# Optimization experiments

Hardware: AMD Instinct MI355X
Metric: run time of the kernel (lower is better)

The kernel has to match this reference:

```python
import jax, jax.numpy as jnp
import numpy as np

NUM_HEADS = 16


def setup_inputs() -> dict:
    key = jax.random.key(0)
    ks = jax.random.split(key, 9)
    B, N, C, R, T = 16, 1024, 1024, 64, 10
    s = 0.02
    x = jax.random.normal(ks[0], (B, N, C), dtype=jnp.float32)
    W_qkv = jax.random.normal(ks[1], (3 * C, C), dtype=jnp.float32) * s
    W_proj = jax.random.normal(ks[2], (C, C), dtype=jnp.float32) * s
    b_proj = jax.random.normal(ks[3], (C,), dtype=jnp.float32) * s
    A_k = jax.random.normal(ks[4], (T, R, C), dtype=jnp.float32) * s
    B_k = jax.random.normal(ks[5], (T, C, R), dtype=jnp.float32) * s
    A_v = jax.random.normal(ks[6], (T, R, C), dtype=jnp.float32) * s
    B_v = jax.random.normal(ks[7], (T, C, R), dtype=jnp.float32) * s
    return {"x": x, "W_qkv": W_qkv, "W_proj": W_proj, "b_proj": b_proj,
            "A_k": A_k, "B_k": B_k, "A_v": A_v, "B_v": B_v, "task": 4}


def reference(x, W_qkv, W_proj, b_proj, A_k, B_k, A_v, B_v, task):
    B, N, C = x.shape
    H = NUM_HEADS
    hd = C // H
    scale = hd ** (-0.5)

    # qkv projection: x @ W_qkv.T -> [B,N,3C] -> [3,B,H,N,hd]
    qkv = (x @ W_qkv.T).reshape(B, N, 3, H, hd).transpose(2, 0, 3, 1, 4)
    q, k, v = qkv[0], qkv[1], qkv[2]

    # merged LoRA weights: sum_{t<=task} B[t] @ A[t] -> [C, C]
    w_k = jnp.einsum('tcr,trd->cd', B_k[:task + 1], A_k[:task + 1])
    w_v = jnp.einsum('tcr,trd->cd', B_v[:task + 1], A_v[:task + 1])
    # F.linear(x, W) = x @ W.T ; reshape to [B,H,N,hd]
    dk = (x @ w_k.T).reshape(B, N, H, hd).transpose(0, 2, 1, 3)
    dv = (x @ w_v.T).reshape(B, N, H, hd).transpose(0, 2, 1, 3)
    k = k + dk
    v = v + dv

    attn = jax.nn.softmax(jnp.einsum('bhnd,bhmd->bhnm', q, k) * scale, axis=-1)
    out = jnp.einsum('bhnm,bhmd->bhnd', attn, v)
    out = out.transpose(0, 2, 1, 3).reshape(B, N, C)
    return out @ W_proj.T + b_proj
```

## Files before the change

kernel.cpp:

```cpp
#include <hip/hip_runtime.h>

typedef __attribute__((ext_vector_type(4))) float f32x4;
typedef __attribute__((ext_vector_type(8))) short s16x8;
typedef __attribute__((ext_vector_type(2))) unsigned int u32x2;
typedef __attribute__((ext_vector_type(4))) unsigned int u32x4;

#define LOG2E 1.44269504088896340736f

__device__ inline unsigned short f2b(float f) {
  unsigned int u = __float_as_uint(f);
  unsigned int r = (u + 0x7FFFu + ((u >> 16) & 1u)) >> 16;
  return (unsigned short)r;
}

__device__ inline unsigned int cvtpk_bf16(float lo, float hi) {
  unsigned int r;
  asm("v_cvt_pk_bf16_f32 %0, %1, %2" : "=v"(r) : "v"(lo), "v"(hi));
  return r;
}

__device__ inline void gload_lds16(const unsigned short* g, unsigned short* l) {
  __builtin_amdgcn_global_load_lds(
      (const __attribute__((address_space(1))) unsigned int*)g,
      (__attribute__((address_space(3))) unsigned int*)l, 16, 0, 0);
}

#define MFMA16(a, b, c) __builtin_amdgcn_mfma_f32_16x16x32_bf16((a), (b), (c), 0, 0, 0)

__global__ __launch_bounds__(256) void lora_and_cvt(const float* __restrict__ A_k,
                                                    const float* __restrict__ B_k,
                                                    const float* __restrict__ A_v,
                                                    const float* __restrict__ B_v,
                                                    float* __restrict__ wk,
                                                    float* __restrict__ wv,
                                                    const int* __restrict__ taskp,
                                                    const float* __restrict__ x,
                                                    const float* __restrict__ Wproj,
                                                    unsigned short* __restrict__ xb,
                                                    unsigned short* __restrict__ Wp) {
  __shared__ float Bs[64][65];
  __shared__ float As[64][65];
  const int blk = blockIdx.x;
  const int tid = threadIdx.x;
  if (blk >= 512) {
    int i = (blk - 512) * 256 + tid;
    const float* src;
    unsigned short* dst;
    int idx;
    if (i < 4194304) { idx = i; src = x; dst = xb; }
    else { idx = i - 4194304; src = Wproj; dst = Wp; }
    f32x4 v = ((const f32x4*)src)[idx];
    unsigned short o0 = f2b(v.x), o1 = f2b(v.y), o2 = f2b(v.z), o3 = f2b(v.w);
    unsigned long long pack = (unsigned long long)o0 | ((unsigned long long)o1 << 16) |
                              ((unsigned long long)o2 << 32) | ((unsigned long long)o3 << 48);
    ((unsigned long long*)dst)[idx] = pack;
    return;
  }
  const int kv = (blk >> 8) & 1;
  const float* A_ = kv ? A_v : A_k;
  const float* B_ = kv ? B_v : B_k;
  float* Wd = kv ? wv : wk;
  const int tile = blk & 255;
  const int c0 = (tile >> 4) * 64, d0 = (tile & 15) * 64;
  const int tx = tid & 15, ty = tid >> 4;
  const int T = *taskp + 1;
  float acc[4][4] = {};
  const int r = tid >> 2, cb = (tid & 3) * 16;
  for (int t = 0; t < T; ++t) {
    __syncthreads();
    const float* srcB = B_ + (size_t)t * 65536 + (size_t)(c0 + r) * 64 + cb;
    const float* srcA = A_ + (size_t)t * 65536 + (size_t)r * 1024 + d0 + cb;
#pragma unroll
    for (int j = 0; j < 16; j += 4) {
      f32x4 vb = *(const f32x4*)(srcB + j);
      Bs[r][cb + j] = vb.x; Bs[r][cb + j + 1] = vb.y;
      Bs[r][cb + j + 2] = vb.z; Bs[r][cb + j + 3] = vb.w;
      f32x4 va = *(const f32x4*)(srcA + j);
      As[r][cb + j] = va.x; As[r][cb + j + 1] = va.y;
      As[r][cb + j + 2] = va.z; As[r][cb + j + 3] = va.w;
    }
    __syncthreads();
#pragma unroll 8
    for (int rr = 0; rr < 64; ++rr) {
      float bv[4], av[4];
#pragma unroll
      for (int i2 = 0; i2 < 4; ++i2) bv[i2] = Bs[ty * 4 + i2][rr];
#pragma unroll
      for (int j = 0; j < 4; ++j) av[j] = As[rr][tx * 4 + j];
#pragma unroll
      for (int i2 = 0; i2 < 4; ++i2)
#pragma unroll
        for (int j = 0; j < 4; ++j) acc[i2][j] += bv[i2] * av[j];
    }
  }
#pragma unroll
  for (int i2 = 0; i2 < 4; ++i2)
#pragma unroll
    for (int j = 0; j < 4; ++j)
      Wd[(size_t)(c0 + ty * 4 + i2) * 1024 + d0 + tx * 4 + j] = acc[i2][j];
}

__global__ void build_wc(const float* __restrict__ Wqkv, const float* __restrict__ wk,
                         const float* __restrict__ wv, unsigned short* __restrict__ Wc) {
  int i = blockIdx.x * 256 + threadIdx.x;
  int e = i * 4;
  f32x4 v = *(const f32x4*)(Wqkv + e);
  int row = e >> 10;
  if (row >= 2048) {
    f32x4 d = *(const f32x4*)(wv + (e - 2097152));
    v = v + d;
  } else if (row >= 1024) {
    f32x4 d = *(const f32x4*)(wk + (e - 1048576));
    v = v + d;
  }
  unsigned short o0 = f2b(v.x), o1 = f2b(v.y), o2 = f2b(v.z), o3 = f2b(v.w);
  unsigned long long pack = (unsigned long long)o0 | ((unsigned long long)o1 << 16) |
                            ((unsigned long long)o2 << 32) | ((unsigned long long)o3 << 48);
  ((unsigned long long*)Wc)[i] = pack;
}

template <int OUT_BF16, int ADD_BIAS, int VFUSE>
__global__ __launch_bounds__(512, 1) void gemm256(const unsigned short* __restrict__ A,
                                                  const unsigned short* __restrict__ B,
                                                  void* __restrict__ Cout,
                                                  const float* __restrict__ bias,
                                                  unsigned short* __restrict__ Vt,
                                                  int M, int N, int K) {
  __shared__ unsigned short SM[65536];
  const int tid = threadIdx.x;
  const int w = tid >> 6, l = tid & 63;
  const int lr = l & 15, lg = l >> 4;
  const int wm = w >> 2, wn = w & 3;

  const int lin = blockIdx.y * gridDim.x + blockIdx.x;
  const int cpx = (gridDim.x * gridDim.y) >> 3;
  const int s = (lin & 7) * cpx + (lin >> 3);
  const int bx = s % gridDim.x, by = s / gridDim.x;

  const int r_st = tid >> 2;
  const int k_st = ((tid & 3) ^ ((tid >> 3) & 3)) << 3;
  const unsigned short* gA0 = A + (size_t)(by * 256 + r_st) * K + k_st;
  const unsigned short* gA1 = A + (size_t)(by * 256 + 128 + r_st) * K + k_st;
  const unsigned short* gB0 = B + (size_t)(bx * 256 + r_st) * K + k_st;
  const unsigned short* gB1 = B + (size_t)(bx * 256 + 128 + r_st) * K + k_st;
  const int wb = w * 512;

  const int fs = lr * 32 + ((lg ^ ((lr >> 1) & 3)) << 3);
  const int A0 = wm * 8192;
  const int B0 = 32768 + (wn >> 1) * 8192;
  const int nb = (wn & 1) * 4;

  f32x4 acc[8][4] = {};
  const int NT2 = K >> 7;

#define STA(bb, kt, kk)                                                          \
  gload_lds16(gA0 + (kt) * 64 + (kk) * 32, &SM[(bb) * 16384 + (kk) * 4096 + wb]); \
  gload_lds16(gA1 + (kt) * 64 + (kk) * 32, &SM[(bb) * 16384 + 8192 + (kk) * 4096 + wb]);
#define STB(bb, kt, kk)                                                                   \
  gload_lds16(gB0 + (kt) * 64 + (kk) * 32, &SM[32768 + (bb) * 16384 + (kk) * 4096 + wb]); \
  gload_lds16(gB1 + (kt) * 64 + (kk) * 32, &SM[32768 + (bb) * 16384 + 8192 + (kk) * 4096 + wb]);
#define PH_GATE                                            \
  __builtin_amdgcn_s_barrier();                            \
  asm volatile("s_waitcnt lgkmcnt(0)" ::: "memory");       \
  __builtin_amdgcn_sched_barrier(0);                       \
  __builtin_amdgcn_s_setprio(1);
#define PH_END                                             \
  __builtin_amdgcn_s_setprio(0);                           \
  __builtin_amdgcn_sched_barrier(0);                       \
  __builtin_amdgcn_s_barrier();
#define PH_END_VM                                          \
  __builtin_amdgcn_s_setprio(0);                           \
  __builtin_amdgcn_sched_barrier(0);                       \
  asm volatile("s_waitcnt vmcnt(6)" ::: "memory");         \
  __builtin_amdgcn_s_barrier();                            \
  __builtin_amdgcn_sched_barrier(0);

  STA(0, 0, 0); STB(0, 0, 0); STA(0, 0, 1); STB(0, 0, 1);
  STA(1, 1, 0); STB(1, 1, 0); STA(1, 1, 1);
  asm volatile("s_waitcnt vmcnt(6)" ::: "memory");
  __builtin_amdgcn_s_barrier();
  __builtin_amdgcn_sched_barrier(0);

  for (int it = 0; it < NT2; ++it) {
    const int kt1 = 2 * it + 1;
    const int st2 = (it < NT2 - 1) ? 2 * it + 2 : 2 * it;
    const int st3 = (it < NT2 - 1) ? 2 * it + 3 : 2 * it + 1;
    s16x8 af[8], bf[2];
#pragma unroll
    for (int m = 0; m < 8; ++m) af[m] = *(const s16x8*)&SM[A0 + m * 512 + fs];
#pragma unroll
    for (int j = 0; j < 2; ++j) bf[j] = *(const s16x8*)&SM[B0 + (nb + j) * 512 + fs];
    STB(1, kt1, 1);
    PH_GATE
#pragma unroll
    for (int m = 0; m < 8; ++m)
#pragma unroll
      for (int j = 0; j < 2; ++j) acc[m][j] = MFMA16(af[m], bf[j], acc[m][j]);
    PH_END
#pragma unroll
    for (int j = 0; j < 2; ++j) bf[j] = *(const s16x8*)&SM[B0 + (nb + 2 + j) * 512 + fs];
    STA(0, st2, 0);
    PH_GATE
#pragma unroll
    for (int m = 0; m < 8; ++m)
#pragma unroll
      for (int j = 0; j < 2; ++j) acc[m][2 + j] = MFMA16(af[m], bf[j], acc[m][2 + j]);
    PH_END
#pragma unroll
    for (int m = 0; m < 8; ++m) af[m] = *(const s16x8*)&SM[A0 + 4096 + m * 512 + fs];
#pragma unroll
    for (int j = 0; j < 2; ++j) bf[j] = *(const s16x8*)&SM[B0 + 4096 + (nb + j) * 512 + fs];
    STB(0, st2, 0);
    PH_GATE
#pragma unroll
    for (int m = 0; m < 8; ++m)
#pragma unroll
      for (int j = 0; j < 2; ++j) acc[m][j] = MFMA16(af[m], bf[j], acc[m][j]);
    PH_END
#pragma unroll
    for (int j = 0; j < 2; ++j) bf[j] = *(const s16x8*)&SM[B0 + 4096 + (nb + 2 + j) * 512 + fs];
    STA(0, st2, 1);
    PH_GATE
#pragma unroll
    for (int m = 0; m < 8; ++m)
#pragma unroll
      for (int j = 0; j < 2; ++j) acc[m][2 + j] = MFMA16(af[m], bf[j], acc[m][2 + j]);
    PH_END_VM
#pragma unroll
    for (int m = 0; m < 8; ++m) af[m] = *(const s16x8*)&SM[16384 + A0 + m * 512 + fs];
#pragma unroll
    for (int j = 0; j < 2; ++j) bf[j] = *(const s16x8*)&SM[16384 + B0 + (nb + j) * 512 + fs];
    STB(0, st2, 1);
    PH_GATE
#pragma unroll
    for (int m = 0; m < 8; ++m)
#pragma unroll
      for (int j = 0; j < 2; ++j) acc[m][j] = MFMA16(af[m], bf[j], acc[m][j]);
    PH_END
#pragma unroll
    for (int j = 0; j < 2; ++j) bf[j] = *(const s16x8*)&SM[16384 + B0 + (nb + 2 + j) * 512 + fs];
    STA(1, st3, 0);
    PH_GATE
#pragma unroll
    for (int m = 0; m < 8; ++m)
#pragma unroll
      for (int j = 0; j < 2; ++j) acc[m][2 + j] = MFMA16(af[m], bf[j], acc[m][2 + j]);
    PH_END
#pragma unroll
    for (int m = 0; m < 8; ++m) af[m] = *(const s16x8*)&SM[16384 + A0 + 4096 + m * 512 + fs];
#pragma unroll
    for (int j = 0; j < 2; ++j) bf[j] = *(const s16x8*)&SM[16384 + B0 + 4096 + (nb + j) * 512 + fs];
    STB(1, st3, 0);
    PH_GATE
#pragma unroll
    for (int m = 0; m < 8; ++m)
#pragma unroll
      for (int j = 0; j < 2; ++j) acc[m][j] = MFMA16(af[m], bf[j], acc[m][j]);
    PH_END
#pragma unroll
    for (int j = 0; j < 2; ++j) bf[j] = *(const s16x8*)&SM[16384 + B0 + 4096 + (nb + 2 + j) * 512 + fs];
    STA(1, st3, 1);
    PH_GATE
#pragma unroll
    for (int m = 0; m < 8; ++m)
#pragma unroll
      for (int j = 0; j < 2; ++j) acc[m][2 + j] = MFMA16(af[m], bf[j], acc[m][2 + j]);
    PH_END_VM
  }

  const int crow0 = by * 256 + wm * 128;
  const int ccol0 = bx * 256 + wn * 64;

  if (VFUSE) {
    unsigned short* Cq = (unsigned short*)Cout;
    if (bx < 8) {
      unsigned short* Cb = Cq + ((size_t)((ccol0 >> 10) & 1)) * 16777216;
#pragma unroll
      for (int m = 0; m < 8; ++m)
#pragma unroll
        for (int n = 0; n < 4; ++n)
#pragma unroll
          for (int rr = 0; rr < 4; ++rr) {
            int row = crow0 + m * 16 + lg * 4 + rr;
            int col = (ccol0 + n * 16 + lr) & 1023;
            Cb[(size_t)row * 1024 + col] = f2b(acc[m][n][rr]);
          }
    } else {
      asm volatile("s_waitcnt vmcnt(0)" ::: "memory");
      __syncthreads();
      unsigned int* T32 = (unsigned int*)SM;
      const int h0 = (bx - 8) * 4;
      const int bb = by >> 2;
      const int n_base = (by & 3) * 256;
#pragma unroll
      for (int hf = 0; hf < 2; ++hf) {
        if (wm == hf) {
#pragma unroll
          for (int m = 0; m < 8; ++m)
#pragma unroll
            for (int n = 0; n < 4; ++n) {
              int lcol = wn * 64 + n * 16 + lr;
              u32x2 pk;
              pk.x = (unsigned int)f2b(acc[m][n][0]) | ((unsigned int)f2b(acc[m][n][1]) << 16);
              pk.y = (unsigned int)f2b(acc[m][n][2]) | ((unsigned int)f2b(acc[m][n][3]) << 16);
              *(u32x2*)&T32[lcol * 68 + m * 8 + lg * 2] = pk;
            }
        }
        __syncthreads();
#pragma unroll
        for (int p = 0; p < 8; ++p) {
          int slot2 = p * 512 + tid;
          int d256 = slot2 >> 4;
          int ncq = (slot2 & 15) * 4;
          u32x4 v = *(const u32x4*)&T32[d256 * 68 + ncq];
          int hloc = d256 >> 6, d = d256 & 63;
          size_t dst = (size_t)(bb * 16 + h0 + hloc) * 65536 + (size_t)d * 1024 +
                       (n_base + hf * 128 + ncq * 2);
          *(u32x4*)&Vt[dst] = v;
        }
        __syncthreads();
      }
    }
  } else if (OUT_BF16) {
    unsigned short* C = (unsigned short*)Cout;
#pragma unroll
    for (int m = 0; m < 8; ++m)
#pragma unroll
      for (int n = 0; n < 4; ++n)
#pragma unroll
        for (int rr = 0; rr < 4; ++rr) {
          int row = crow0 + m * 16 + lg * 4 + rr;
          int col = ccol0 + n * 16 + lr;
          C[(size_t)row * N + col] = f2b(acc[m][n][rr]);
        }
  } else {
    float* C = (float*)Cout;
#pragma unroll
    for (int m = 0; m < 8; ++m)
#pragma unroll
      for (int n = 0; n < 4; ++n)
#pragma unroll
        for (int rr = 0; rr < 4; ++rr) {
          int row = crow0 + m * 16 + lg * 4 + rr;
          int col = ccol0 + n * 16 + lr;
          float b = ADD_BIAS ? bias[col] : 0.f;
          C[(size_t)row * N + col] = acc[m][n][rr] + b;
        }
  }
#undef STA
#undef STB
#undef PH_GATE
#undef PH_END
#undef PH_END_VM
}

__global__ __launch_bounds__(512) void attn_fwd(const unsigned short* __restrict__ Qb,
                                                const unsigned short* __restrict__ Kb,
                                                const unsigned short* __restrict__ vT,
                                                unsigned short* __restrict__ out) {
  const int tid = threadIdx.x;
  const int w = tid >> 6, l = tid & 63;
  const int lr = l & 15, lg = l >> 4;
  const int bid = blockIdx.x;
  const int g = (bid & 7) * 32 + (bid >> 5);
  const int qt2 = (bid >> 3) & 3;
  const int b = g >> 4, h = g & 15;

  __shared__ unsigned short Ks[2][4096];
  __shared__ unsigned short Vs[2][4096];
  __shared__ unsigned int Ps[8][576];

  const size_t base = (size_t)b * 1048576 + h * 64;
  const unsigned short* Qp = Qb + base;
  const unsigned short* Kp = Kb + base;
  const unsigned short* vTp = vT + (size_t)(b * 16 + h) * 65536;

  const float SSCALE = 0.125f * LOG2E;
  const int qb = qt2 * 256;
  s16x8 qf[2][2];
#pragma unroll
  for (int qg = 0; qg < 2; ++qg) {
    const int qrow = qb + qg * 128 + w * 16 + lr;
    qf[qg][0] = *(const s16x8*)(Qp + (size_t)qrow * 1024 + lg * 8);
    qf[qg][1] = *(const s16x8*)(Qp + (size_t)qrow * 1024 + 32 + lg * 8);
#pragma unroll
    for (int kk = 0; kk < 2; ++kk)
#pragma unroll
      for (int j = 0; j < 8; ++j) {
        float f = __uint_as_float(((unsigned int)(unsigned short)qf[qg][kk][j]) << 16) * SSCALE;
        qf[qg][kk][j] = (short)f2b(f);
      }
  }

  s16x8 ONES;
#pragma unroll
  for (int j = 0; j < 8; ++j) ONES[j] = (short)0x3F80;

  f32x4 o[2][4] = {};
  f32x4 o4[2] = {};

  const int srow = tid >> 3;
  const int csrc = (tid & 7) ^ (srow & 7);

  gload_lds16(Kp + (size_t)srow * 1024 + csrc * 8, &Ks[0][w * 512]);
  gload_lds16(vTp + (size_t)srow * 1024 + csrc * 8, &Vs[0][w * 512]);
  __syncthreads();

  for (int t = 0; t < 16; ++t) {
    const int cur = t & 1;
    if (t < 15) {
      const int kv1 = (t + 1) * 64;
      gload_lds16(Kp + (size_t)(kv1 + srow) * 1024 + csrc * 8, &Ks[cur ^ 1][w * 512]);
      gload_lds16(vTp + (size_t)srow * 1024 + kv1 + csrc * 8, &Vs[cur ^ 1][w * 512]);
    }
    const unsigned short* Kb_ = &Ks[cur][0];
    const unsigned short* Vb = &Vs[cur][0];

    f32x4 sc[2][4] = {};
    __builtin_amdgcn_s_setprio(1);
#pragma unroll
    for (int kk = 0; kk < 2; ++kk)
#pragma unroll
      for (int tt = 0; tt < 4; ++tt) {
        int krow = tt * 16 + lr;
        s16x8 kf = *(const s16x8*)&Kb_[krow * 64 + ((((kk * 32 + lg * 8) >> 3) ^ (krow & 7)) << 3)];
        sc[0][tt] = MFMA16(kf, qf[0][kk], sc[0][tt]);
        sc[1][tt] = MFMA16(kf, qf[1][kk], sc[1][tt]);
      }
    __builtin_amdgcn_s_setprio(0);

    s16x8 pf[2][2];
#pragma unroll
    for (int qg = 0; qg < 2; ++qg) {
      unsigned int* Pw = &Ps[w][0];
#pragma unroll
      for (int tt = 0; tt < 4; ++tt) {
        float p0 = exp2f(sc[qg][tt][0]);
        float p1 = exp2f(sc[qg][tt][1]);
        float p2 = exp2f(sc[qg][tt][2]);
        float p3 = exp2f(sc[qg][tt][3]);
        u32x2 pk;
        pk.x = cvtpk_bf16(p0, p1);
        pk.y = cvtpk_bf16(p2, p3);
        *(u32x2*)&Pw[lr * 36 + tt * 8 + lg * 2] = pk;
      }
      __builtin_amdgcn_sched_barrier(0);
#pragma unroll
      for (int kk = 0; kk < 2; ++kk) {
        u32x4 pu = *(const u32x4*)&Pw[lr * 36 + kk * 16 + lg * 4];
        pf[qg][kk] = __builtin_bit_cast(s16x8, pu);
      }
      __builtin_amdgcn_sched_barrier(0);
    }

#pragma unroll
    for (int kk = 0; kk < 2; ++kk) {
      __builtin_amdgcn_s_setprio(1);
      o4[0] = MFMA16(pf[0][kk], ONES, o4[0]);
      o4[1] = MFMA16(pf[1][kk], ONES, o4[1]);
#pragma unroll
      for (int dt = 0; dt < 4; ++dt) {
        int vrow = dt * 16 + lr;
        s16x8 vf = *(const s16x8*)&Vb[vrow * 64 + ((((kk * 32 + lg * 8) >> 3) ^ (vrow & 7)) << 3)];
        o[0][dt] = MFMA16(pf[0][kk], vf, o[0][dt]);
        o[1][dt] = MFMA16(pf[1][kk], vf, o[1][dt]);
      }
      __builtin_amdgcn_s_setprio(0);
    }
    __syncthreads();
  }

#pragma unroll
  for (int qg = 0; qg < 2; ++qg) {
    f32x4 lq;
#pragma unroll
    for (int rr = 0; rr < 4; ++rr) lq[rr] = 1.f / o4[qg][rr];
    const size_t orow0 = (size_t)b * 1024 + qb + qg * 128 + w * 16;
#pragma unroll
    for (int dt = 0; dt < 4; ++dt)
#pragma unroll
      for (int rr = 0; rr < 4; ++rr)
        out[(orow0 + lg * 4 + rr) * 1024 + h * 64 + dt * 16 + lr] = f2b(o[qg][dt][rr] * lq[rr]);
  }
}

extern "C" void kernel_launch(void* const* d_in, const int* in_sizes, int n_in,
                              void* d_out, int out_size, void* d_ws, size_t ws_size,
                              hipStream_t stream) {
  const float* x = (const float*)d_in[0];
  const float* Wqkv = (const float*)d_in[1];
  const float* Wproj = (const float*)d_in[2];
  const float* bproj = (const float*)d_in[3];
  const float* A_k = (const float*)d_in[4];
  const float* B_k = (const float*)d_in[5];
  const float* A_v = (const float*)d_in[6];
  const float* B_v = (const float*)d_in[7];
  const int* task = (const int*)d_in[8];

  char* ws = (char*)d_ws;
  float* wk = (float*)ws;
  float* wv = (float*)(ws + (4ull << 20));
  unsigned short* xb = (unsigned short*)(ws + (8ull << 20));
  unsigned short* Wc = (unsigned short*)(ws + (40ull << 20));
  unsigned short* Wp = (unsigned short*)(ws + (46ull << 20));
  unsigned short* Qb = (unsigned short*)(ws + (48ull << 20));
  unsigned short* Kb = (unsigned short*)(ws + (80ull << 20));
  unsigned short* vT = (unsigned short*)(ws + (112ull << 20));
  unsigned short* ao = (unsigned short*)(ws + (144ull << 20));

  lora_and_cvt<<<17920, 256, 0, stream>>>(A_k, B_k, A_v, B_v, wk, wv, task, x, Wproj, xb, Wp);
  build_wc<<<3072, 256, 0, stream>>>(Wqkv, wk, wv, Wc);
  gemm256<1, 0, 1><<<dim3(12, 64), 512, 0, stream>>>(xb, Wc, Qb, nullptr, vT, 16384, 3072, 1024);
  attn_fwd<<<1024, 512, 0, stream>>>(Qb, Kb, vT, ao);
  gemm256<0, 1, 0><<<dim3(4, 64), 512, 0, stream>>>(ao, Wp, d_out, bproj, nullptr, 16384, 1024, 1024);
}
```

Before: 299.8 us.

## Load GEMM B operand directly from global into registers, bypassing LDS

The GEMM kernel no longer stages the B tile through shared memory. Each wave loads its own B fragments straight from global memory into double-buffered registers (bfA/bfB), and the vmcnt waits are retuned to match. This removes the LDS writes and reads for B and halves LDS usage, but it raises register pressure and makes the waves sharing a B column load the same data redundantly, without coalescing through LDS.

```diff
diff --git a/kernel.cpp b/kernel.cpp
--- a/kernel.cpp
+++ b/kernel.cpp
@@ -126,7 +126,7 @@
                                                   const float* __restrict__ bias,
                                                   unsigned short* __restrict__ Vt,
                                                   int M, int N, int K) {
-  __shared__ unsigned short SM[65536];
+  __shared__ unsigned short SM[34816];
   const int tid = threadIdx.x;
   const int w = tid >> 6, l = tid & 63;
   const int lr = l & 15, lg = l >> 4;
@@ -141,24 +141,29 @@
   const int k_st = ((tid & 3) ^ ((tid >> 3) & 3)) << 3;
   const unsigned short* gA0 = A + (size_t)(by * 256 + r_st) * K + k_st;
   const unsigned short* gA1 = A + (size_t)(by * 256 + 128 + r_st) * K + k_st;
-  const unsigned short* gB0 = B + (size_t)(bx * 256 + r_st) * K + k_st;
-  const unsigned short* gB1 = B + (size_t)(bx * 256 + 128 + r_st) * K + k_st;
   const int wb = w * 512;
 
   const int fs = lr * 32 + ((lg ^ ((lr >> 1) & 3)) << 3);
   const int A0 = wm * 8192;
-  const int B0 = 32768 + (wn >> 1) * 8192;
-  const int nb = (wn & 1) * 4;
+
+  const unsigned short* gBw =
+      B + (size_t)(bx * 256 + (wn >> 1) * 128 + (wn & 1) * 64 + lr) * K + lg * 8;
 
   f32x4 acc[8][4] = {};
   const int NT2 = K >> 7;
 
-#define STA(bb, kt, kk)                                                          \
+#define STA(bb, kt, kk)                                                           \
   gload_lds16(gA0 + (kt) * 64 + (kk) * 32, &SM[(bb) * 16384 + (kk) * 4096 + wb]); \
   gload_lds16(gA1 + (kt) * 64 + (kk) * 32, &SM[(bb) * 16384 + 8192 + (kk) * 4096 + wb]);
-#define STB(bb, kt, kk)                                                                   \
-  gload_lds16(gB0 + (kt) * 64 + (kk) * 32, &SM[32768 + (bb) * 16384 + (kk) * 4096 + wb]); \
-  gload_lds16(gB1 + (kt) * 64 + (kk) * 32, &SM[32768 + (bb) * 16384 + 8192 + (kk) * 4096 + wb]);
+#define LDB(dst, kt)                                                        \
+  dst[0][0] = *(const s16x8*)(gBw + 0 * (size_t)K + (kt) * 64);             \
+  dst[0][1] = *(const s16x8*)(gBw + 0 * (size_t)K + (kt) * 64 + 32);        \
+  dst[1][0] = *(const s16x8*)(gBw + 16 * (size_t)K + (kt) * 64);            \
+  dst[1][1] = *(const s16x8*)(gBw + 16 * (size_t)K + (kt) * 64 + 32);       \
+  dst[2][0] = *(const s16x8*)(gBw + 32 * (size_t)K + (kt) * 64);            \
+  dst[2][1] = *(const s16x8*)(gBw + 32 * (size_t)K + (kt) * 64 + 32);       \
+  dst[3][0] = *(const s16x8*)(gBw + 48 * (size_t)K + (kt) * 64);            \
+  dst[3][1] = *(const s16x8*)(gBw + 48 * (size_t)K + (kt) * 64 + 32);
 #define PH_GATE                                            \
   __builtin_amdgcn_s_barrier();                            \
   asm volatile("s_waitcnt lgkmcnt(0)" ::: "memory");       \
@@ -171,13 +176,15 @@
 #define PH_END_VM                                          \
   __builtin_amdgcn_s_setprio(0);                           \
   __builtin_amdgcn_sched_barrier(0);                       \
-  asm volatile("s_waitcnt vmcnt(6)" ::: "memory");         \
+  asm volatile("s_waitcnt vmcnt(4)" ::: "memory");         \
   __builtin_amdgcn_s_barrier();                            \
   __builtin_amdgcn_sched_barrier(0);
 
-  STA(0, 0, 0); STB(0, 0, 0); STA(0, 0, 1); STB(0, 0, 1);
-  STA(1, 1, 0); STB(1, 1, 0); STA(1, 1, 1);
-  asm volatile("s_waitcnt vmcnt(6)" ::: "memory");
+  s16x8 bfA[4][2], bfB[4][2];
+
+  STA(0, 0, 0); STA(0, 0, 1); STA(1, 1, 0); STA(1, 1, 1);
+  LDB(bfA, 0);
+  asm volatile("s_waitcnt vmcnt(8)" ::: "memory");
   __builtin_amdgcn_s_barrier();
   __builtin_amdgcn_sched_barrier(0);
 
@@ -185,86 +192,68 @@
     const int kt1 = 2 * it + 1;
     const int st2 = (it < NT2 - 1) ? 2 * it + 2 : 2 * it;
     const int st3 = (it < NT2 - 1) ? 2 * it + 3 : 2 * it + 1;
-    s16x8 af[8], bf[2];
+    s16x8 af[8];
 #pragma unroll
     for (int m = 0; m < 8; ++m) af[m] = *(const s16x8*)&SM[A0 + m * 512 + fs];
-#pragma unroll
-    for (int j = 0; j < 2; ++j) bf[j] = *(const s16x8*)&SM[B0 + (nb + j) * 512 + fs];
-    STB(1, kt1, 1);
-    PH_GATE
-#pragma unroll
-    for (int m = 0; m < 8; ++m)
-#pragma unroll
-      for (int j = 0; j < 2; ++j) acc[m][j] = MFMA16(af[m], bf[j], acc[m][j]);
+    LDB(bfB, kt1);
+    PH_GATE
+#pragma unroll
+    for (int m = 0; m < 8; ++m)
+#pragma unroll
+      for (int j = 0; j < 2; ++j) acc[m][j] = MFMA16(af[m], bfA[j][0], acc[m][j]);
     PH_END
-#pragma unroll
-    for (int j = 0; j < 2; ++j) bf[j] = *(const s16x8*)&SM[B0 + (nb + 2 + j) * 512 + fs];
     STA(0, st2, 0);
     PH_GATE
 #pragma unroll
     for (int m = 0; m < 8; ++m)
 #pragma unroll
-      for (int j = 0; j < 2; ++j) acc[m][2 + j] = MFMA16(af[m], bf[j], acc[m][2 + j]);
+      for (int j = 0; j < 2; ++j) acc[m][2 + j] = MFMA16(af[m], bfA[2 + j][0], acc[m][2 + j]);
     PH_END
 #pragma unroll
     for (int m = 0; m < 8; ++m) af[m] = *(const s16x8*)&SM[A0 + 4096 + m * 512 + fs];
-#pragma unroll
-    for (int j = 0; j < 2; ++j) bf[j] = *(const s16x8*)&SM[B0 + 4096 + (nb + j) * 512 + fs];
-    STB(0, st2, 0);
-    PH_GATE
-#pragma unroll
-    for (int m = 0; m < 8; ++m)
-#pragma unroll
-      for (int j = 0; j < 2; ++j) acc[m][j] = MFMA16(af[m], bf[j], acc[m][j]);
+    PH_GATE
+#pragma unroll
+    for (int m = 0; m < 8; ++m)
+#pragma unroll
+      for (int j = 0; j < 2; ++j) acc[m][j] = MFMA16(af[m], bfA[j][1], acc[m][j]);
     PH_END
-#pragma unroll
-    for (int j = 0; j < 2; ++j) bf[j] = *(const s16x8*)&SM[B0 + 4096 + (nb + 2 + j) * 512 + fs];
     STA(0, st2, 1);
     PH_GATE
 #pragma unroll
     for (int m = 0; m < 8; ++m)
 #pragma unroll
-      for (int j = 0; j < 2; ++j) acc[m][2 + j] = MFMA16(af[m], bf[j], acc[m][2 + j]);
+      for (int j = 0; j < 2; ++j) acc[m][2 + j] = MFMA16(af[m], bfA[2 + j][1], acc[m][2 + j]);
     PH_END_VM
 #pragma unroll
     for (int m = 0; m < 8; ++m) af[m] = *(const s16x8*)&SM[16384 + A0 + m * 512 + fs];
-#pragma unroll
-    for (int j = 0; j < 2; ++j) bf[j] = *(const s16x8*)&SM[16384 + B0 + (nb + j) * 512 + fs];
-    STB(0, st2, 1);
-    PH_GATE
-#pragma unroll
-    for (int m = 0; m < 8; ++m)
-#pragma unroll
-      for (int j = 0; j < 2; ++j) acc[m][j] = MFMA16(af[m], bf[j], acc[m][j]);
+    LDB(bfA, st2);
+    PH_GATE
+#pragma unroll
+    for (int m = 0; m < 8; ++m)
+#pragma unroll
+      for (int j = 0; j < 2; ++j) acc[m][j] = MFMA16(af[m], bfB[j][0], acc[m][j]);
     PH_END
-#pragma unroll
-    for (int j = 0; j < 2; ++j) bf[j] = *(const s16x8*)&SM[16384 + B0 + (nb + 2 + j) * 512 + fs];
     STA(1, st3, 0);
     PH_GATE
 #pragma unroll
     for (int m = 0; m < 8; ++m)
 #pragma unroll
-      for (int j = 0; j < 2; ++j) acc[m][2 + j] = MFMA16(af[m], bf[j], acc[m][2 + j]);
+      for (int j = 0; j < 2; ++j) acc[m][2 + j] = MFMA16(af[m], bfB[2 + j][0], acc[m][2 + j]);
     PH_END
 #pragma unroll
     for (int m = 0; m < 8; ++m) af[m] = *(const s16x8*)&SM[16384 + A0 + 4096 + m * 512 + fs];
-#pragma unroll
-    for (int j = 0; j < 2; ++j) bf[j] = *(const s16x8*)&SM[16384 + B0 + 4096 + (nb + j) * 512 + fs];
-    STB(1, st3, 0);
-    PH_GATE
-#pragma unroll
-    for (int m = 0; m < 8; ++m)
-#pragma unroll
-      for (int j = 0; j < 2; ++j) acc[m][j] = MFMA16(af[m], bf[j], acc[m][j]);
+    PH_GATE
+#pragma unroll
+    for (int m = 0; m < 8; ++m)
+#pragma unroll
+      for (int j = 0; j < 2; ++j) acc[m][j] = MFMA16(af[m], bfB[j][1], acc[m][j]);
     PH_END
-#pragma unroll
-    for (int j = 0; j < 2; ++j) bf[j] = *(const s16x8*)&SM[16384 + B0 + 4096 + (nb + 2 + j) * 512 + fs];
     STA(1, st3, 1);
     PH_GATE
 #pragma unroll
     for (int m = 0; m < 8; ++m)
 #pragma unroll
-      for (int j = 0; j < 2; ++j) acc[m][2 + j] = MFMA16(af[m], bf[j], acc[m][2 + j]);
+      for (int j = 0; j < 2; ++j) acc[m][2 + j] = MFMA16(af[m], bfB[2 + j][1], acc[m][2 + j]);
     PH_END_VM
   }
 
@@ -348,7 +337,7 @@
         }
   }
 #undef STA
-#undef STB
+#undef LDB
 #undef PH_GATE
 #undef PH_END
 #undef PH_END_VM
```

New measurement: 358.9 us. +19.7%, slower.
